# Performance work log

Measured on AMD Instinct MI355X. Metric: run time of the kernel, lower is better.

## Reference

```python
import jax, jax.numpy as jnp
import numpy as np

MARGIN = 0.3
ANCHOR = 0.5
EPS = 1e-8  # torch F.cosine_similarity default eps


def _cosine(a, b):
    # a: [N, D], b: [D] -> [N]
    num = a @ b
    den = jnp.maximum(jnp.linalg.norm(a, axis=-1) * jnp.linalg.norm(b), EPS)
    return num / den


def setup_inputs() -> dict:
    key = jax.random.key(0)
    k1, k2, k3, k4 = jax.random.split(key, 4)
    N, D = 8192, 1024
    return {
        "q_emb": jax.random.normal(k1, (D,), dtype=jnp.float32),
        "d_embs": jax.random.normal(k2, (N, D), dtype=jnp.float32),
        "c_emb": jax.random.normal(k3, (D,), dtype=jnp.float32),
        "rates": jax.random.uniform(k4, (N,), dtype=jnp.float32),
    }


def reference(q_emb, d_embs, c_emb, rates):
    # cosine similarity of each distractor vs question / correct answer
    s_q = _cosine(d_embs, q_emb)          # [N]
    _s_c = _cosine(d_embs, c_emb)         # [N] computed in original, never used
    quality = jnp.abs(rates - ANCHOR)     # [N]

    # Vectorized form of the nested i,j loop:
    # pair (i, j) contributes relu(margin + s_q[j] - s_q[i]) iff quality[i] > quality[j]
    mask = quality[:, None] > quality[None, :]              # [N, N]; diagonal is False
    pair_loss = jax.nn.relu(MARGIN + s_q[None, :] - s_q[:, None])  # [N, N]
    total = jnp.sum(jnp.where(mask, pair_loss, jnp.float32(0.0)))
    n_pairs = jnp.sum(mask)
    return total / jnp.maximum(n_pairs, 1).astype(total.dtype)
```

## Files before the change

kernel.cpp:

```cpp
#include <hip/hip_runtime.h>

#define MARGIN 0.3f
#define ANCHOR 0.5f
#define EPS    1e-8f
#define BJ     256
#define NSLOT  32

typedef unsigned long long ull;


__global__ __launch_bounds__(256) void sq_kernel(
        const float* __restrict__ q, const float* __restrict__ d,
        const float* __restrict__ rates,
        float* __restrict__ sq, float* __restrict__ qual,
        char* __restrict__ acc, int N, int D) {
    int tid = threadIdx.x;
    if (blockIdx.x == 0) {
        if (tid < NSLOT)              *(double*)  (acc + (size_t)tid * 64)               = 0.0;
        else if (tid < 2 * NSLOT)     *(unsigned*)(acc + 2048 + (size_t)(tid - 32) * 64) = 0u;
        else if (tid < 3 * NSLOT)     *(unsigned*)(acc + 4096 + (size_t)(tid - 64) * 64) = 0u;
        else if (tid == 3 * NSLOT)    *(unsigned*)(acc + 6144)                           = 0u;
    }
    int wave = (blockIdx.x * blockDim.x + tid) >> 6;
    int lane = tid & 63;
    if (wave >= N) return;
    const float* row = d + (size_t)wave * (size_t)D;

    float dot = 0.f, dn = 0.f, qn = 0.f;
    for (int it = lane * 4; it < D; it += 256) {
        float4 dv = *(const float4*)(row + it);
        float4 qv = *(const float4*)(q + it);
        dot += dv.x * qv.x + dv.y * qv.y + dv.z * qv.z + dv.w * qv.w;
        dn  += dv.x * dv.x + dv.y * dv.y + dv.z * dv.z + dv.w * dv.w;
        qn  += qv.x * qv.x + qv.y * qv.y + qv.z * qv.z + qv.w * qv.w;
    }
    #pragma unroll
    for (int off = 32; off >= 1; off >>= 1) {
        dot += __shfl_xor(dot, off);
        dn  += __shfl_xor(dn,  off);
        qn  += __shfl_xor(qn,  off);
    }
    if (lane == 0) {
        float den = fmaxf(sqrtf(dn) * sqrtf(qn), EPS);
        sq[wave]   = dot / den;
        qual[wave] = fabsf(rates[wave] - ANCHOR);
    }
}

__global__ __launch_bounds__(256) void pair_kernel(
        const float* __restrict__ sq, const float* __restrict__ qual,
        int N, char* __restrict__ acc, float* __restrict__ out, unsigned nblocks) {
    __shared__ double   bsum[4];
    __shared__ unsigned bcnt[4];

    int tid = threadIdx.x;
    int i   = blockIdx.x * blockDim.x + tid;
    int j0  = blockIdx.y * BJ;

    float my_sq = (i < N) ? sq[i]   : 0.f;
    float my_q  = (i < N) ? qual[i] : -1.f;
    float a     = MARGIN - my_sq;

    float sum = 0.f;
    unsigned c = 0;
    int jmax = N - j0; if (jmax > BJ) jmax = BJ;

    if (jmax == BJ) {
        const float4* sq4 = (const float4*)(sq   + j0);
        const float4* qu4 = (const float4*)(qual + j0);
        #pragma unroll 8
        for (int j = 0; j < BJ / 4; ++j) {
            float4 sv = sq4[j];
            float4 qv = qu4[j];
            bool m0 = my_q > qv.x;  float v0 = fmaxf(a + sv.x, 0.f);
            bool m1 = my_q > qv.y;  float v1 = fmaxf(a + sv.y, 0.f);
            bool m2 = my_q > qv.z;  float v2 = fmaxf(a + sv.z, 0.f);
            bool m3 = my_q > qv.w;  float v3 = fmaxf(a + sv.w, 0.f);
            sum += m0 ? v0 : 0.f;   c += m0;
            sum += m1 ? v1 : 0.f;   c += m1;
            sum += m2 ? v2 : 0.f;   c += m2;
            sum += m3 ? v3 : 0.f;   c += m3;
        }
    } else {
        for (int j = 0; j < jmax; ++j) {
            bool  m = my_q > qual[j0 + j];
            float v = fmaxf(a + sq[j0 + j], 0.f);
            sum += m ? v : 0.f;
            c   += m ? 1u : 0u;
        }
    }

    #pragma unroll
    for (int off = 32; off >= 1; off >>= 1) {
        sum += __shfl_xor(sum, off);
        c   += __shfl_xor(c,   off);
    }
    int w = tid >> 6;
    if ((tid & 63) == 0) { bsum[w] = (double)sum; bcnt[w] = c; }
    __syncthreads();

    if (tid >= 64) return;

    unsigned last = 0;
    if (tid == 0) {
        double   bs = bsum[0] + bsum[1] + bsum[2] + bsum[3];
        unsigned bc = bcnt[0] + bcnt[1] + bcnt[2] + bcnt[3];
        unsigned bid = blockIdx.y * gridDim.x + blockIdx.x;
        unsigned s   = bid & (NSLOT - 1);

        double   old  = atomicAdd((double*)  (acc + (size_t)s * 64), bs);
        unsigned oldc = atomicAdd((unsigned*)(acc + 2048 + (size_t)s * 64), bc);
        asm volatile("" :: "v"(__double2hiint(old)), "v"(__double2loint(old)), "v"(oldc));

        unsigned gsz = (nblocks > s) ? ((nblocks - 1u - s) / NSLOT + 1u) : 0u;
        unsigned pa  = atomicAdd((unsigned*)(acc + 4096 + (size_t)s * 64), 1u);
        if (pa == gsz - 1u) {
            asm volatile("" :: "v"(pa));
            unsigned nslots = (nblocks < NSLOT) ? nblocks : NSLOT;
            unsigned pm = atomicAdd((unsigned*)(acc + 6144), 1u);
            last = (pm == nslots - 1u) ? 1u : 0u;
        }
    }
    last = __shfl(last, 0);
    if (last) {
        double s = 0.0; ull c2 = 0ull;
        if (tid < NSLOT) {
            s  = atomicAdd((double*)  (acc + (size_t)tid * 64), 0.0);
            c2 = (ull)atomicAdd((unsigned*)(acc + 2048 + (size_t)tid * 64), 0u);
        }
        #pragma unroll
        for (int off = 16; off >= 1; off >>= 1) {
            s  += __shfl_xor(s,  off);
            c2 += __shfl_xor(c2, off);
        }
        if (tid == 0) {
            if (c2 < 1ull) c2 = 1ull;
            out[0] = (float)(s / (double)c2);
        }
    }
}

extern "C" void kernel_launch(void* const* d_in, const int* in_sizes, int n_in,
                              void* d_out, int out_size, void* d_ws, size_t ws_size,
                              hipStream_t stream) {
    const float* q_emb  = (const float*)d_in[0];
    const float* d_embs = (const float*)d_in[1];
    const float* rates  = (const float*)d_in[3];

    int D = in_sizes[0];
    int N = in_sizes[3];

    char*  acc  = (char*)d_ws;
    float* sq   = (float*)(acc + 8192);
    float* qual = sq + N;
    float* out  = (float*)d_out;

    int rows_per_block = 256 / 64;
    sq_kernel<<<(N + rows_per_block - 1) / rows_per_block, 256, 0, stream>>>(
        q_emb, d_embs, rates, sq, qual, acc, N, D);

    dim3 grid((N + 255) / 256, (N + BJ - 1) / BJ);
    pair_kernel<<<grid, 256, 0, stream>>>(sq, qual, N, acc, out,
                                          grid.x * grid.y);
}
```

Baseline: 25.43 us.

## Grid-stride sq rows with q cached in registers; widen pair j-tile

The cosine kernel now launches a quarter as many blocks. Each wave loops over several rows, keeping the q vector and its norm in registers and fully unrolling the 1024-wide dot product as four float4 loads. This removes the repeated q loads and loop overhead per row. The pair kernel's j-tile grows from 256 to 512, halving the block count and the atomic traffic, at the cost of fewer blocks in flight. The code now hardcodes D=1024, so it breaks for other dimensions.

Result: slower. 27.69 us (+8.9%).

```diff
diff --git a/kernel.cpp b/kernel.cpp
--- a/kernel.cpp
+++ b/kernel.cpp
@@ -3,7 +3,6 @@
 #define MARGIN 0.3f
 #define ANCHOR 0.5f
 #define EPS    1e-8f
-#define BJ     256
 #define NSLOT  32
 
 typedef unsigned long long ull;
@@ -21,32 +20,52 @@
         else if (tid < 3 * NSLOT)     *(unsigned*)(acc + 4096 + (size_t)(tid - 64) * 64) = 0u;
         else if (tid == 3 * NSLOT)    *(unsigned*)(acc + 6144)                           = 0u;
     }
-    int wave = (blockIdx.x * blockDim.x + tid) >> 6;
-    int lane = tid & 63;
-    if (wave >= N) return;
-    const float* row = d + (size_t)wave * (size_t)D;
+    const int lane  = tid & 63;
+    const int wid   = (blockIdx.x * blockDim.x + tid) >> 6;
+    const int nwav  = (gridDim.x * blockDim.x) >> 6;
+    const int it0   = lane * 4;
 
-    float dot = 0.f, dn = 0.f, qn = 0.f;
-    for (int it = lane * 4; it < D; it += 256) {
-        float4 dv = *(const float4*)(row + it);
-        float4 qv = *(const float4*)(q + it);
-        dot += dv.x * qv.x + dv.y * qv.y + dv.z * qv.z + dv.w * qv.w;
-        dn  += dv.x * dv.x + dv.y * dv.y + dv.z * dv.z + dv.w * dv.w;
-        qn  += qv.x * qv.x + qv.y * qv.y + qv.z * qv.z + qv.w * qv.w;
-    }
-    #pragma unroll
-    for (int off = 32; off >= 1; off >>= 1) {
-        dot += __shfl_xor(dot, off);
-        dn  += __shfl_xor(dn,  off);
-        qn  += __shfl_xor(qn,  off);
-    }
-    if (lane == 0) {
-        float den = fmaxf(sqrtf(dn) * sqrtf(qn), EPS);
-        sq[wave]   = dot / den;
-        qual[wave] = fabsf(rates[wave] - ANCHOR);
+    float4 q0 = *(const float4*)(q + it0);
+    float4 q1 = *(const float4*)(q + it0 + 256);
+    float4 q2 = *(const float4*)(q + it0 + 512);
+    float4 q3 = *(const float4*)(q + it0 + 768);
+    float qn  = q0.x*q0.x + q0.y*q0.y + q0.z*q0.z + q0.w*q0.w
+              + q1.x*q1.x + q1.y*q1.y + q1.z*q1.z + q1.w*q1.w
+              + q2.x*q2.x + q2.y*q2.y + q2.z*q2.z + q2.w*q2.w
+              + q3.x*q3.x + q3.y*q3.y + q3.z*q3.z + q3.w*q3.w;
+
+    for (int row = wid; row < N; row += nwav) {
+        const float* r = d + (size_t)row * (size_t)D;
+        float4 d0 = *(const float4*)(r + it0);
+        float4 d1 = *(const float4*)(r + it0 + 256);
+        float4 d2 = *(const float4*)(r + it0 + 512);
+        float4 d3 = *(const float4*)(r + it0 + 768);
+
+        float dot = d0.x*q0.x + d0.y*q0.y + d0.z*q0.z + d0.w*q0.w
+                  + d1.x*q1.x + d1.y*q1.y + d1.z*q1.z + d1.w*q1.w
+                  + d2.x*q2.x + d2.y*q2.y + d2.z*q2.z + d2.w*q2.w
+                  + d3.x*q3.x + d3.y*q3.y + d3.z*q3.z + d3.w*q3.w;
+        float dn  = d0.x*d0.x + d0.y*d0.y + d0.z*d0.z + d0.w*d0.w
+                  + d1.x*d1.x + d1.y*d1.y + d1.z*d1.z + d1.w*d1.w
+                  + d2.x*d2.x + d2.y*d2.y + d2.z*d2.z + d2.w*d2.w
+                  + d3.x*d3.x + d3.y*d3.y + d3.z*d3.z + d3.w*d3.w;
+
+        float dq = dot, dd = dn, qq = qn;
+        #pragma unroll
+        for (int off = 32; off >= 1; off >>= 1) {
+            dq += __shfl_xor(dq, off);
+            dd += __shfl_xor(dd, off);
+            qq += __shfl_xor(qq, off);
+        }
+        if (lane == 0) {
+            float den = fmaxf(sqrtf(dd) * sqrtf(qq), EPS);
+            sq[row]   = dq / den;
+            qual[row] = fabsf(rates[row] - ANCHOR);
+        }
     }
 }
 
+#define BJR 512
 __global__ __launch_bounds__(256) void pair_kernel(
         const float* __restrict__ sq, const float* __restrict__ qual,
         int N, char* __restrict__ acc, float* __restrict__ out, unsigned nblocks) {
@@ -55,21 +74,21 @@
 
     int tid = threadIdx.x;
     int i   = blockIdx.x * blockDim.x + tid;
-    int j0  = blockIdx.y * BJ;
+    int j0  = blockIdx.y * BJR;
 
     float my_sq = (i < N) ? sq[i]   : 0.f;
     float my_q  = (i < N) ? qual[i] : -1.f;
     float a     = MARGIN - my_sq;
 
-    float sum = 0.f;
-    unsigned c = 0;
-    int jmax = N - j0; if (jmax > BJ) jmax = BJ;
+    float    sum = 0.f;
+    unsigned c   = 0;
+    int jmax = N - j0; if (jmax > BJR) jmax = BJR;
 
-    if (jmax == BJ) {
+    if ((jmax & 3) == 0) {
         const float4* sq4 = (const float4*)(sq   + j0);
         const float4* qu4 = (const float4*)(qual + j0);
         #pragma unroll 8
-        for (int j = 0; j < BJ / 4; ++j) {
+        for (int j = 0; j < jmax / 4; ++j) {
             float4 sv = sq4[j];
             float4 qv = qu4[j];
             bool m0 = my_q > qv.x;  float v0 = fmaxf(a + sv.x, 0.f);
@@ -155,11 +174,10 @@
     float* qual = sq + N;
     float* out  = (float*)d_out;
 
-    int rows_per_block = 256 / 64;
-    sq_kernel<<<(N + rows_per_block - 1) / rows_per_block, 256, 0, stream>>>(
-        q_emb, d_embs, rates, sq, qual, acc, N, D);
+    int nblk1 = (N + 15) / 16;
+    sq_kernel<<<nblk1, 256, 0, stream>>>(q_emb, d_embs, rates, sq, qual, acc, N, D);
 
-    dim3 grid((N + 255) / 256, (N + BJ - 1) / BJ);
+    dim3 grid((N + 255) / 256, (N + BJR - 1) / BJR);
     pair_kernel<<<grid, 256, 0, stream>>>(sq, qual, N, acc, out,
                                           grid.x * grid.y);
 }
```
